# Performance work log

Measured on AMD Instinct MI355X. Metric: run time of the kernel, lower is better.

Reference implementation:

```python
import jax, jax.numpy as jnp
import numpy as np

D_MODEL = 256   # dim // 2
DIM = 512
D_INNER = 512   # expand=2 * d_model
D_STATE = 16
D_CONV = 4
DT_RANK = 16    # ceil(d_model/16)
N_LAYERS = 2
H_RES, W_RES = 16, 16
EPS = 1e-5


def silu(v):
    return v * jax.nn.sigmoid(v)


def setup_inputs() -> dict:
    key = jax.random.key(0)
    ks = jax.random.split(key, 12)
    Bsz, T, N = 2, 4, 256
    x = jax.random.normal(ks[0], (Bsz, 1 + T * N, DIM), jnp.float32)
    skip = jax.random.normal(ks[1], (Bsz, 1 + 4 * T * N, D_MODEL), jnp.float32)
    sc = lambda k, shape, s: jax.random.normal(k, shape, jnp.float32) * s
    exp_w = sc(ks[2], (2 * DIM, DIM), 0.02)            # PatchExpanding2D.expansion (no bias)
    ln_g = jnp.ones((DIM // 2,), jnp.float32)
    ln_b = jnp.zeros((DIM // 2,), jnp.float32)
    cls_w = sc(ks[3], (DIM // 2, DIM), 0.02)
    cls_b = jnp.zeros((DIM // 2,), jnp.float32)
    in_proj_w = sc(ks[4], (N_LAYERS, 2 * D_INNER, D_MODEL), 0.02)
    conv_w = sc(ks[5], (N_LAYERS, D_INNER, D_CONV), 0.1)  # depthwise causal conv
    conv_b = jnp.zeros((N_LAYERS, D_INNER), jnp.float32)
    xproj_w = sc(ks[6], (N_LAYERS, DT_RANK + 2 * D_STATE, D_INNER), 0.02)
    dt_w = sc(ks[7], (N_LAYERS, D_INNER, DT_RANK), 0.1)
    dt_b = sc(ks[8], (N_LAYERS, D_INNER), 0.1)
    A_log = jnp.log(jnp.broadcast_to(jnp.arange(1, D_STATE + 1, dtype=jnp.float32), (N_LAYERS, D_INNER, D_STATE)))
    Dp = jnp.ones((N_LAYERS, D_INNER), jnp.float32)
    out_w = sc(ks[9], (N_LAYERS, D_MODEL, D_INNER), 0.02)
    bn_g = jnp.ones((D_MODEL,), jnp.float32)
    bn_b = jnp.zeros((D_MODEL,), jnp.float32)
    return {"x": x, "skip_connection": skip, "exp_w": exp_w, "ln_g": ln_g, "ln_b": ln_b,
            "cls_w": cls_w, "cls_b": cls_b, "in_proj_w": in_proj_w, "conv_w": conv_w,
            "conv_b": conv_b, "xproj_w": xproj_w, "dt_w": dt_w, "dt_b": dt_b,
            "A_log": A_log, "Dp": Dp, "out_w": out_w, "bn_g": bn_g, "bn_b": bn_b,
            "B": 2, "T": 4, "N": 256}


def mamba_layer(u, Wi, cw, cb, Wx, Wdt, bdt, A_log, Dd, Wo):
    # u: [B, L, d_model]
    Bb, L, _ = u.shape
    xz = jnp.einsum('bld,ed->ble', u, Wi)            # [B, L, 2*d_inner]
    xi, z = jnp.split(xz, 2, axis=-1)
    # depthwise causal conv1d (pad left d_conv-1)
    xp = jnp.pad(xi, ((0, 0), (D_CONV - 1, 0), (0, 0)))
    xc = cb + sum(cw[:, k] * xp[:, k:k + L, :] for k in range(D_CONV))
    xi = silu(xc)
    dbc = jnp.einsum('bld,ed->ble', xi, Wx)          # [B, L, dt_rank + 2*d_state]
    dt = dbc[..., :DT_RANK]
    Bm = dbc[..., DT_RANK:DT_RANK + D_STATE]
    Cm = dbc[..., DT_RANK + D_STATE:]
    delta = jax.nn.softplus(jnp.einsum('blr,dr->bld', dt, Wdt) + bdt)  # [B, L, d_inner]
    A = -jnp.exp(A_log)                              # [d_inner, d_state]

    def step(h, inp):
        d_t, B_t, C_t, x_t = inp                     # [B,d], [B,n], [B,n], [B,d]
        h = h * jnp.exp(d_t[..., None] * A) + d_t[..., None] * B_t[:, None, :] * x_t[..., None]
        y = jnp.einsum('bdn,bn->bd', h, C_t)
        return h, y

    h0 = jnp.zeros((Bb, D_INNER, D_STATE), u.dtype)
    xs = (jnp.swapaxes(delta, 0, 1), jnp.swapaxes(Bm, 0, 1),
          jnp.swapaxes(Cm, 0, 1), jnp.swapaxes(xi, 0, 1))
    _, ys = jax.lax.scan(step, h0, xs)               # ys: [L, B, d_inner]
    y = jnp.swapaxes(ys, 0, 1) + xi * Dd
    y = y * silu(z)
    return jnp.einsum('bld,od->blo', y, Wo)          # [B, L, d_model]


def reference(x, skip_connection, exp_w, ln_g, ln_b, cls_w, cls_b, in_proj_w, conv_w,
              conv_b, xproj_w, dt_w, dt_b, A_log, Dp, out_w, bn_g, bn_b, B, T, N):
    cls = x[:B, :1, :]                               # [B, 1, dim]
    toks = x[:, 1:, :].reshape(x.shape[0], T, N, DIM)
    # patch expanding: Linear dim -> 2*dim, then 2x2 pixel shuffle, LayerNorm(dim//2)
    e = jnp.einsum('btnm,em->btne', toks, exp_w)     # [B, T, N, 2*dim]
    m = (2 * DIM) // 4                               # dim // 2
    e = e.reshape(-1, T, H_RES, W_RES, 2, 2, m)
    e = jnp.transpose(e, (0, 1, 2, 4, 3, 5, 6)).reshape(-1, T, 4 * N, m)
    mu = e.mean(-1, keepdims=True)
    var = e.var(-1, keepdims=True)
    e = (e - mu) / jnp.sqrt(var + EPS) * ln_g + ln_b
    e = e.reshape(e.shape[0], T * 4 * N, m)
    cls = jnp.einsum('bom,em->boe', cls, cls_w) + cls_b
    xx = jnp.concatenate([cls, e], axis=1) + skip_connection
    for i in range(N_LAYERS):
        xx = mamba_layer(xx, in_proj_w[i], conv_w[i], conv_b[i], xproj_w[i],
                         dt_w[i], dt_b[i], A_log[i], Dp[i], out_w[i])
    # BatchNorm1d over channels (training-mode batch stats, biased variance)
    mu = xx.mean(axis=(0, 1))
    var = xx.var(axis=(0, 1))
    xx = (xx - mu) / jnp.sqrt(var + EPS) * bn_g + bn_b
    return xx, 4 * N
```

## Files before the change

kernel.cpp:

```cpp
#include <hip/hip_runtime.h>
#include <hip/hip_bf16.h>
#include <math.h>

#define L_TOT 4097
#define BSZ 2
#define ROWS (BSZ*L_TOT)
#define NSEG 128
#define SEGLEN 33

typedef __bf16 bf16x8 __attribute__((ext_vector_type(8)));
typedef float  f32x4  __attribute__((ext_vector_type(4)));
#define ASTR 56
#define AST2 72

__device__ __forceinline__ float sigmoidf_(float v){ return 1.0f/(1.0f+__expf(-v)); }
__device__ __forceinline__ float siluf_(float v){ return v * sigmoidf_(v); }
__device__ __forceinline__ unsigned short bfbits(float f){
    __bf16 h = (__bf16)f;
    return __builtin_bit_cast(unsigned short, h);
}

__global__ __launch_bounds__(256) void cvt4(
    const float* __restrict__ w0, const float* __restrict__ w1,
    const float* __restrict__ w2, const float* __restrict__ w3,
    __bf16* __restrict__ o0, __bf16* __restrict__ o1,
    __bf16* __restrict__ o2, __bf16* __restrict__ o3)
{
    long i = ((long)blockIdx.x*256 + threadIdx.x)*8;
    const float* src; __bf16* dst; long off;
    if (i < 524288)        { src = w0; dst = o0; off = i; }
    else if (i < 1048576)  { src = w1; dst = o1; off = i - 524288; }
    else if (i < 1310720)  { src = w2; dst = o2; off = i - 1048576; }
    else if (i < 1359872)  { src = w3; dst = o3; off = i - 1310720; }
    else return;
    float4 a = *(const float4*)(src+off), b = *(const float4*)(src+off+4);
    bf16x8 o;
    o[0]=(__bf16)a.x; o[1]=(__bf16)a.y; o[2]=(__bf16)a.z; o[3]=(__bf16)a.w;
    o[4]=(__bf16)b.x; o[5]=(__bf16)b.y; o[6]=(__bf16)b.z; o[7]=(__bf16)b.w;
    *(bf16x8*)(dst+off) = o;
}

__global__ __launch_bounds__(256) void cvt_gather_x(
    const float* __restrict__ x, __bf16* __restrict__ out)
{
    long i = ((long)blockIdx.x*256 + threadIdx.x)*8;
    if (i >= 2048L*512) return;
    int row = (int)(i >> 9), col = (int)(i & 511);
    long srow = row + (row >> 10) + 1;
    const float* src = x + srow*512 + col;
    float4 a = *(const float4*)src, b = *(const float4*)(src+4);
    bf16x8 o;
    o[0]=(__bf16)a.x; o[1]=(__bf16)a.y; o[2]=(__bf16)a.z; o[3]=(__bf16)a.w;
    o[4]=(__bf16)b.x; o[5]=(__bf16)b.y; o[6]=(__bf16)b.z; o[7]=(__bf16)b.w;
    *(bf16x8*)(out+i) = o;
}

__global__ __launch_bounds__(256) void gemm_bf16(
    const __bf16* __restrict__ A, const __bf16* __restrict__ W,
    __bf16* __restrict__ C2, int M, int N, int K)
{
    __shared__ __bf16 Als[128*ASTR];
    __shared__ __bf16 Wls[64*ASTR];
    const int tid = threadIdx.x;
    const int lane = tid & 63, w = tid >> 6;
    const int n0 = blockIdx.x*64, m0 = blockIdx.y*128;

    f32x4 acc[2][4] = {};
    const int arow = tid >> 1, ahalf = tid & 1;
    const int wrow = tid >> 2, wseg = tid & 3;
    const int fr = lane & 15, fc = lane >> 4;

    for (int k0 = 0; k0 < K; k0 += 32) {
        bf16x8 av0 = {}, av1 = {};
        if (m0 + arow < M) {
            const __bf16* src = A + (long)(m0+arow)*K + k0 + ahalf*16;
            av0 = *(const bf16x8*)src;
            av1 = *(const bf16x8*)(src+8);
        }
        bf16x8 wv = *(const bf16x8*)(W + (long)(n0+wrow)*K + k0 + wseg*8);
        __syncthreads();
        *(bf16x8*)&Als[arow*ASTR + ahalf*16]     = av0;
        *(bf16x8*)&Als[arow*ASTR + ahalf*16 + 8] = av1;
        *(bf16x8*)&Wls[wrow*ASTR + wseg*8]       = wv;
        __syncthreads();

        bf16x8 a0 = *(const bf16x8*)&Als[(w*32 +      fr)*ASTR + fc*8];
        bf16x8 a1 = *(const bf16x8*)&Als[(w*32 + 16 + fr)*ASTR + fc*8];
        #pragma unroll
        for (int j = 0; j < 4; j++) {
            bf16x8 bv = *(const bf16x8*)&Wls[(j*16 + fr)*ASTR + fc*8];
            acc[0][j] = __builtin_amdgcn_mfma_f32_16x16x32_bf16(a0, bv, acc[0][j], 0,0,0);
            acc[1][j] = __builtin_amdgcn_mfma_f32_16x16x32_bf16(a1, bv, acc[1][j], 0,0,0);
        }
    }
    #pragma unroll
    for (int i = 0; i < 2; i++) {
        #pragma unroll
        for (int rr = 0; rr < 4; rr++) {
            int grow = m0 + w*32 + i*16 + fc*4 + rr;
            if (grow < M) {
                #pragma unroll
                for (int j = 0; j < 4; j++)
                    C2[(long)grow*N + n0 + j*16 + fr] = (__bf16)acc[i][j][rr];
            }
        }
    }
}

__global__ __launch_bounds__(256) void gemm_inproj(
    const __bf16* __restrict__ A, const __bf16* __restrict__ W,
    __bf16* __restrict__ xhb, __bf16* __restrict__ zsb, int M, int K)
{
    __shared__ __bf16 Als[128*AST2];
    __shared__ __bf16 Wls[128*AST2];
    const int tid = threadIdx.x;
    const int lane = tid & 63, w = tid >> 6;
    const int n0 = blockIdx.x*128, m0 = blockIdx.y*128;
    const int fr = lane & 15, fc = lane >> 4;
    const int row2 = tid >> 1, half = tid & 1;

    f32x4 acc[2][8] = {};

    for (int k0 = 0; k0 < K; k0 += 64) {
        bf16x8 av[4], wv[4];
        const bool aok = (m0 + row2) < M;
        const __bf16* asrc = A + (long)(m0+row2)*K + k0 + half*32;
        const __bf16* wsrc = W + (long)(n0+row2)*K + k0 + half*32;
        #pragma unroll
        for (int e = 0; e < 4; e++) {
            av[e] = aok ? *(const bf16x8*)(asrc + e*8) : (bf16x8){};
            wv[e] = *(const bf16x8*)(wsrc + e*8);
        }
        __syncthreads();
        #pragma unroll
        for (int e = 0; e < 4; e++) {
            *(bf16x8*)&Als[row2*AST2 + half*32 + e*8] = av[e];
            *(bf16x8*)&Wls[row2*AST2 + half*32 + e*8] = wv[e];
        }
        __syncthreads();
        #pragma unroll
        for (int s = 0; s < 2; s++) {
            bf16x8 a0 = *(const bf16x8*)&Als[(w*32 +      fr)*AST2 + s*32 + fc*8];
            bf16x8 a1 = *(const bf16x8*)&Als[(w*32 + 16 + fr)*AST2 + s*32 + fc*8];
            #pragma unroll
            for (int j = 0; j < 8; j++) {
                bf16x8 bv = *(const bf16x8*)&Wls[(j*16 + fr)*AST2 + s*32 + fc*8];
                acc[0][j] = __builtin_amdgcn_mfma_f32_16x16x32_bf16(a0, bv, acc[0][j], 0,0,0);
                acc[1][j] = __builtin_amdgcn_mfma_f32_16x16x32_bf16(a1, bv, acc[1][j], 0,0,0);
            }
        }
    }
    const bool xhalf = (n0 < 512);
    const int cbase = xhalf ? n0 : (n0 - 512);
    #pragma unroll
    for (int i = 0; i < 2; i++) {
        #pragma unroll
        for (int rr = 0; rr < 4; rr++) {
            int grow = m0 + w*32 + i*16 + fc*4 + rr;
            if (grow < M) {
                if (xhalf) {
                    #pragma unroll
                    for (int j = 0; j < 8; j++)
                        xhb[(long)grow*512 + cbase + j*16 + fr] = (__bf16)acc[i][j][rr];
                } else {
                    #pragma unroll
                    for (int j = 0; j < 8; j++)
                        zsb[(long)grow*512 + cbase + j*16 + fr] = (__bf16)siluf_(acc[i][j][rr]);
                }
            }
        }
    }
}

__global__ __launch_bounds__(128) void gemm_dbc(
    const __bf16* __restrict__ A, const __bf16* __restrict__ W,
    float* __restrict__ dt16, float* __restrict__ BC, int M)
{
    __shared__ __bf16 Als[64*ASTR];
    __shared__ __bf16 Wls[48*ASTR];
    const int tid = threadIdx.x;
    const int lane = tid & 63, w = tid >> 6;
    const int m0 = blockIdx.x*64;
    f32x4 acc[2][3] = {};

    const int arow = tid >> 1, ahalf = tid & 1;
    const int fr = lane & 15, fc = lane >> 4;

    for (int k0 = 0; k0 < 512; k0 += 32) {
        bf16x8 av0 = {}, av1 = {};
        if (m0 + arow < M) {
            const __bf16* src = A + (long)(m0+arow)*512 + k0 + ahalf*16;
            av0 = *(const bf16x8*)src;
            av1 = *(const bf16x8*)(src+8);
        }
        bf16x8 wv0 = {}, wv1 = {};
        if (tid < 96) {
            const __bf16* src = W + (long)(tid>>1)*512 + k0 + (tid&1)*16;
            wv0 = *(const bf16x8*)src;
            wv1 = *(const bf16x8*)(src+8);
        }
        __syncthreads();
        *(bf16x8*)&Als[arow*ASTR + ahalf*16]     = av0;
        *(bf16x8*)&Als[arow*ASTR + ahalf*16 + 8] = av1;
        if (tid < 96) {
            *(bf16x8*)&Wls[(tid>>1)*ASTR + (tid&1)*16]     = wv0;
            *(bf16x8*)&Wls[(tid>>1)*ASTR + (tid&1)*16 + 8] = wv1;
        }
        __syncthreads();

        bf16x8 a0 = *(const bf16x8*)&Als[(w*32 +      fr)*ASTR + fc*8];
        bf16x8 a1 = *(const bf16x8*)&Als[(w*32 + 16 + fr)*ASTR + fc*8];
        #pragma unroll
        for (int j = 0; j < 3; j++) {
            bf16x8 bv = *(const bf16x8*)&Wls[(j*16 + fr)*ASTR + fc*8];
            acc[0][j] = __builtin_amdgcn_mfma_f32_16x16x32_bf16(a0, bv, acc[0][j], 0,0,0);
            acc[1][j] = __builtin_amdgcn_mfma_f32_16x16x32_bf16(a1, bv, acc[1][j], 0,0,0);
        }
    }
    #pragma unroll
    for (int i = 0; i < 2; i++) {
        #pragma unroll
        for (int rr = 0; rr < 4; rr++) {
            long grow = m0 + w*32 + i*16 + fc*4 + rr;
            if (grow < M) {
                dt16[grow*16 + fr]    = acc[i][0][rr];
                BC[grow*32 + fr]      = acc[i][1][rr];
                BC[grow*32 + 16 + fr] = acc[i][2][rr];
            }
        }
    }
}

__global__ __launch_bounds__(256) void delta_k(
    const float* __restrict__ dt16, const float* __restrict__ Wdt,
    const float* __restrict__ bdt, const __bf16* __restrict__ xib,
    unsigned* __restrict__ pdx)
{
    __shared__ float dtS[8*16];
    const int tid = threadIdx.x;
    const long r0 = (long)blockIdx.x*8;
    if (tid < 32) {
        long idx = r0*16 + tid*4;
        f32x4 v = (idx < (long)ROWS*16) ? *(const f32x4*)&dt16[idx] : (f32x4){};
        *(f32x4*)&dtS[tid*4] = v;
    }
    const int d0 = tid, d1 = tid + 256;
    f32x4 wa[4], wb[4];
    #pragma unroll
    for (int q = 0; q < 4; q++) {
        wa[q] = *(const f32x4*)(Wdt + d0*16 + q*4);
        wb[q] = *(const f32x4*)(Wdt + d1*16 + q*4);
    }
    const float b0 = bdt[d0], b1 = bdt[d1];
    __syncthreads();
    #pragma unroll
    for (int rr = 0; rr < 8; rr++) {
        long row = r0 + rr;
        if (row >= ROWS) return;
        const float* dt = &dtS[rr*16];
        float s0 = b0, s1 = b1;
        #pragma unroll
        for (int e = 0; e < 4; e++) {
            s0 += wa[0][e]*dt[e] + wa[1][e]*dt[4+e] + wa[2][e]*dt[8+e] + wa[3][e]*dt[12+e];
            s1 += wb[0][e]*dt[e] + wb[1][e]*dt[4+e] + wb[2][e]*dt[8+e] + wb[3][e]*dt[12+e];
        }
        float dl0 = (s0 > 20.f) ? s0 : log1pf(__expf(s0));
        float dl1 = (s1 > 20.f) ? s1 : log1pf(__expf(s1));
        unsigned x0 = __builtin_bit_cast(unsigned short, xib[row*512 + d0]);
        unsigned x1 = __builtin_bit_cast(unsigned short, xib[row*512 + d1]);
        pdx[row*512 + d0] = (unsigned)bfbits(dl0) | (x0 << 16);
        pdx[row*512 + d1] = (unsigned)bfbits(dl1) | (x1 << 16);
    }
}

__global__ __launch_bounds__(256) void cls_k(
    const float* __restrict__ x, const float* __restrict__ cls_w,
    const float* __restrict__ cls_b, const float* __restrict__ skip,
    __bf16* __restrict__ xxb)
{
    const int widx = blockIdx.x*4 + (threadIdx.x >> 6);
    const int lane = threadIdx.x & 63;
    const int b = widx >> 8, c = widx & 255;
    const float* xr = x + (long)b*1025*512 + lane*8;
    const float* wr = cls_w + (long)c*512 + lane*8;
    float4 xa = *(const float4*)xr,      xb4 = *(const float4*)(xr+4);
    float4 wa = *(const float4*)wr,      wb4 = *(const float4*)(wr+4);
    float s = xa.x*wa.x + xa.y*wa.y + xa.z*wa.z + xa.w*wa.w
            + xb4.x*wb4.x + xb4.y*wb4.y + xb4.z*wb4.z + xb4.w*wb4.w;
    #pragma unroll
    for (int o = 32; o > 0; o >>= 1) s += __shfl_xor(s, o);
    if (lane == 0) {
        long o = (long)b*L_TOT*256 + c;
        xxb[o] = (__bf16)(s + cls_b[c] + skip[o]);
    }
}

__global__ __launch_bounds__(256) void rearrange_ln(
    const __bf16* __restrict__ e_buf, const float* __restrict__ ln_g,
    const float* __restrict__ ln_b, const float* __restrict__ skip,
    __bf16* __restrict__ xxb)
{
    const int wv = threadIdx.x >> 6, lane = threadIdx.x & 63;
    const int qg = blockIdx.x*4 + wv;
    const int b = qg >> 12, q = (qg & 4095) + 1;
    const long obase = ((long)b*L_TOT + q)*256;

    const int t  = (q-1) >> 10;
    const int p  = (q-1) & 1023;
    const int h  = p >> 6;
    const int a  = (p >> 5) & 1;
    const int w_ = (p >> 1) & 15;
    const int bb = p & 1;
    const long tok = (long)b*1024 + t*256 + h*16 + w_;
    const __bf16* src = e_buf + tok*1024 + a*512 + bb*256 + lane*4;
    float v[4];
    {
        ushort2 u0 = *(const ushort2*)src;
        ushort2 u1 = *(const ushort2*)(src+2);
        v[0] = (float)__builtin_bit_cast(__bf16, u0.x);
        v[1] = (float)__builtin_bit_cast(__bf16, u0.y);
        v[2] = (float)__builtin_bit_cast(__bf16, u1.x);
        v[3] = (float)__builtin_bit_cast(__bf16, u1.y);
    }
    float s = v[0]+v[1]+v[2]+v[3];
    float s2 = v[0]*v[0]+v[1]*v[1]+v[2]*v[2]+v[3]*v[3];
    #pragma unroll
    for (int o = 32; o > 0; o >>= 1) { s += __shfl_xor(s, o); s2 += __shfl_xor(s2, o); }
    float mu = s * (1.f/256.f);
    float rs = rsqrtf(s2*(1.f/256.f) - mu*mu + 1e-5f);
    const int c0 = lane*4;
    float4 sk = *(const float4*)&skip[obase + c0];
    float skv[4] = {sk.x, sk.y, sk.z, sk.w};
    __bf16 ov[4];
    #pragma unroll
    for (int i = 0; i < 4; i++)
        ov[i] = (__bf16)((v[i] - mu)*rs*ln_g[c0+i] + ln_b[c0+i] + skv[i]);
    *(ushort2*)&xxb[obase + c0]     = make_ushort2(
        __builtin_bit_cast(unsigned short, ov[0]),
        __builtin_bit_cast(unsigned short, ov[1]));
    *(ushort2*)&xxb[obase + c0 + 2] = make_ushort2(
        __builtin_bit_cast(unsigned short, ov[2]),
        __builtin_bit_cast(unsigned short, ov[3]));
}

__global__ __launch_bounds__(256) void conv_silu(
    const __bf16* __restrict__ xhb, const float* __restrict__ cw,
    const float* __restrict__ cb, __bf16* __restrict__ xib)
{
    const int tid = threadIdx.x;
    const int c = tid & 63;
    const long r0 = ((long)blockIdx.x*4 + (tid >> 6))*8;
    if (r0 >= ROWS) return;
    const int d0 = c*8;
    float wreg[4][8], breg[8];
    #pragma unroll
    for (int e = 0; e < 8; e++) {
        breg[e] = cb[d0+e];
        #pragma unroll
        for (int k = 0; k < 4; k++) wreg[k][e] = cw[(d0+e)*4 + k];
    }
    bf16x8 win[4];
    #pragma unroll
    for (int j = 0; j < 3; j++) {
        long rr = r0 - 3 + j;
        win[j] = (rr >= 0) ? *(const bf16x8*)&xhb[rr*512 + d0] : (bf16x8){};
    }
    #pragma unroll
    for (int rr = 0; rr < 8; rr++) {
        long rl = r0 + rr;
        if (rl >= ROWS) break;
        win[3] = *(const bf16x8*)&xhb[rl*512 + d0];
        int l = (int)(rl % L_TOT);
        float acc[8];
        #pragma unroll
        for (int e = 0; e < 8; e++) acc[e] = breg[e];
        #pragma unroll
        for (int k = 0; k < 4; k++) {
            if (l + k - 3 >= 0) {
                #pragma unroll
                for (int e = 0; e < 8; e++)
                    acc[e] += wreg[k][e]*(float)win[k][e];
            }
        }
        bf16x8 o;
        #pragma unroll
        for (int e = 0; e < 8; e++) o[e] = (__bf16)siluf_(acc[e]);
        *(bf16x8*)&xib[rl*512 + d0] = o;
        win[0] = win[1]; win[1] = win[2]; win[2] = win[3];
    }
}

__global__ __launch_bounds__(256) void scan_p1(
    const unsigned* __restrict__ pdx,
    const float* __restrict__ BC, const float* __restrict__ A_log,
    float* __restrict__ segH, float* __restrict__ segP)
{
    __shared__ unsigned pdxS[SEGLEN*64];
    __shared__ float bS[SEGLEN*16];
    const int blk = blockIdx.x;
    const int seg = blk >> 4;
    const int b   = (blk >> 3) & 1;
    const int dbase = (blk & 7)*64;
    const int tid = threadIdx.x;
    const int l0 = seg*SEGLEN;
    const int nl = min(l0 + SEGLEN, L_TOT) - l0;
    const int nlc = nl > 0 ? nl : 0;

    for (int cc = tid; cc < nlc*16; cc += 256) {
        int l = cc >> 4, qq = cc & 15;
        *(uint4*)&pdxS[l*64 + qq*4] =
            *(const uint4*)&pdx[((long)b*L_TOT + l0 + l)*512 + dbase + qq*4];
    }
    for (int cc = tid; cc < nlc*4; cc += 256) {
        int l = cc >> 2, qq = cc & 3;
        *(f32x4*)&bS[l*16 + qq*4] =
            *(const f32x4*)&BC[((long)b*L_TOT + l0 + l)*32 + qq*4];
    }
    __syncthreads();

    const int dl_ = tid >> 2;
    const int d = dbase + dl_;
    const int ng = tid & 3;
    f32x4 Al = *(const f32x4*)(A_log + d*16 + ng*4);
    float Ar[4] = {-__expf(Al[0]), -__expf(Al[1]), -__expf(Al[2]), -__expf(Al[3])};
    float h[4] = {0,0,0,0};
    float P[4] = {1,1,1,1};
    for (int l = 0; l < nlc; l++) {
        unsigned v = pdxS[l*64 + dl_];
        float dl = __uint_as_float(v << 16);
        float xv = __uint_as_float(v & 0xffff0000u);
        f32x4 Bv = *(const f32x4*)&bS[l*16 + ng*4];
        float dx = dl*xv;
        #pragma unroll
        for (int n = 0; n < 4; n++) {
            float E = __expf(dl*Ar[n]);
            h[n] = h[n]*E + dx*Bv[n];
            P[n] *= E;
        }
    }
    long off = ((long)(seg*2 + b)*512 + d)*16 + ng*4;
    *(f32x4*)&segH[off] = f32x4{h[0],h[1],h[2],h[3]};
    *(f32x4*)&segP[off] = f32x4{P[0],P[1],P[2],P[3]};
}

__global__ __launch_bounds__(256) void scan_p2(
    float* __restrict__ segH, const float* __restrict__ segP)
{
    const int idx = blockIdx.x*256 + threadIdx.x;
    float carry = 0.f;
    for (int s0 = 0; s0 < NSEG; s0 += 8) {
        float hh[8], pp[8];
        #pragma unroll
        for (int j = 0; j < 8; j++) {
            long o = (long)(s0+j)*16384 + idx;
            hh[j] = segH[o]; pp[j] = segP[o];
        }
        #pragma unroll
        for (int j = 0; j < 8; j++) {
            long o = (long)(s0+j)*16384 + idx;
            segH[o] = carry;
            carry = pp[j]*carry + hh[j];
        }
    }
}

__global__ __launch_bounds__(256) void scan_p3(
    const unsigned* __restrict__ pdx,
    const float* __restrict__ BC, const float* __restrict__ A_log,
    const float* __restrict__ segH, const float* __restrict__ Dp,
    const __bf16* __restrict__ zsb, __bf16* __restrict__ yb)
{
    __shared__ unsigned pdxS[SEGLEN*64];
    __shared__ float bcS[SEGLEN*32];
    __shared__ __bf16 zS[SEGLEN*64];
    __shared__ __bf16 yS[SEGLEN*64];
    const int blk = blockIdx.x;
    const int seg = blk >> 4;
    const int b   = (blk >> 3) & 1;
    const int dbase = (blk & 7)*64;
    const int tid = threadIdx.x;
    const int l0 = seg*SEGLEN;
    const int nl = min(l0 + SEGLEN, L_TOT) - l0;
    const int nlc = nl > 0 ? nl : 0;
    if (nlc == 0) return;

    for (int cc = tid; cc < nlc*16; cc += 256) {
        int l = cc >> 4, qq = cc & 15;
        *(uint4*)&pdxS[l*64 + qq*4] =
            *(const uint4*)&pdx[((long)b*L_TOT + l0 + l)*512 + dbase + qq*4];
    }
    for (int cc = tid; cc < nlc*8; cc += 256) {
        int l = cc >> 3, qq = cc & 7;
        *(f32x4*)&bcS[l*32 + qq*4] =
            *(const f32x4*)&BC[((long)b*L_TOT + l0 + l)*32 + qq*4];
    }
    for (int cc = tid; cc < nlc*8; cc += 256) {
        int l = cc >> 3, qq = cc & 7;
        *(bf16x8*)&zS[l*64 + qq*8] =
            *(const bf16x8*)&zsb[((long)b*L_TOT + l0 + l)*512 + dbase + qq*8];
    }
    __syncthreads();

    const int dl_ = tid >> 2;
    const int d = dbase + dl_;
    const int ng = tid & 3;
    f32x4 Al = *(const f32x4*)(A_log + d*16 + ng*4);
    float Ar[4] = {-__expf(Al[0]), -__expf(Al[1]), -__expf(Al[2]), -__expf(Al[3])};
    long off = ((long)(seg*2 + b)*512 + d)*16 + ng*4;
    f32x4 h4 = *(const f32x4*)&segH[off];
    float h[4] = {h4[0], h4[1], h4[2], h4[3]};
    const float Dd = Dp[d];
    for (int l = 0; l < nlc; l++) {
        unsigned v = pdxS[l*64 + dl_];
        float dl = __uint_as_float(v << 16);
        float xv = __uint_as_float(v & 0xffff0000u);
        f32x4 Bv = *(const f32x4*)&bcS[l*32 + ng*4];
        f32x4 Cv = *(const f32x4*)&bcS[l*32 + 16 + ng*4];
        float dx = dl*xv;
        float y = 0.f;
        #pragma unroll
        for (int n = 0; n < 4; n++) {
            float E = __expf(dl*Ar[n]);
            h[n] = h[n]*E + dx*Bv[n];
            y += h[n]*Cv[n];
        }
        y += __shfl_xor(y, 1);
        y += __shfl_xor(y, 2);
        if (ng == 0) {
            float z = (float)zS[l*64 + dl_];
            yS[l*64 + dl_] = (__bf16)((y + xv*Dd)*z);
        }
    }
    __syncthreads();
    for (int cc = tid; cc < nlc*8; cc += 256) {
        int l = cc >> 3, qq = cc & 7;
        *(bf16x8*)&yb[((long)b*L_TOT + l0 + l)*512 + dbase + qq*8] =
            *(bf16x8*)&yS[l*64 + qq*8];
    }
}

__global__ void zero_stats(float* __restrict__ stats) { stats[threadIdx.x] = 0.f; }

__global__ __launch_bounds__(256) void bn_reduce(
    const __bf16* __restrict__ xxb, float* __restrict__ stats)
{
    const int c = threadIdx.x;
    float s = 0.f, s2 = 0.f;
    for (int r = blockIdx.x; r < ROWS; r += gridDim.x) {
        float v = (float)xxb[(long)r*256 + c];
        s += v; s2 += v*v;
    }
    atomicAdd(&stats[c], s);
    atomicAdd(&stats[256 + c], s2);
}

__global__ __launch_bounds__(256) void bn_apply(
    const __bf16* __restrict__ xxb, const float* __restrict__ stats,
    const float* __restrict__ g, const float* __restrict__ bta,
    float* __restrict__ out)
{
    long idx = (long)blockIdx.x*256 + threadIdx.x;
    if (idx == 0) out[(long)ROWS*256] = 1024.0f;
    if (idx >= (long)ROWS*256) return;
    int c = (int)(idx & 255);
    float mu = stats[c] * (1.f/ROWS);
    float var = stats[256 + c] * (1.f/ROWS) - mu*mu;
    out[idx] = ((float)xxb[idx] - mu)*rsqrtf(var + 1e-5f)*g[c] + bta[c];
}

extern "C" void kernel_launch(void* const* d_in, const int* in_sizes, int n_in,
                              void* d_out, int out_size, void* d_ws, size_t ws_size,
                              hipStream_t stream)
{
    const float* x        = (const float*)d_in[0];
    const float* skip     = (const float*)d_in[1];
    const float* exp_w    = (const float*)d_in[2];
    const float* ln_g     = (const float*)d_in[3];
    const float* ln_b     = (const float*)d_in[4];
    const float* cls_w    = (const float*)d_in[5];
    const float* cls_b    = (const float*)d_in[6];
    const float* in_proj_w= (const float*)d_in[7];
    const float* conv_w   = (const float*)d_in[8];
    const float* conv_b   = (const float*)d_in[9];
    const float* xproj_w  = (const float*)d_in[10];
    const float* dt_w     = (const float*)d_in[11];
    const float* dt_b     = (const float*)d_in[12];
    const float* A_log    = (const float*)d_in[13];
    const float* Dp       = (const float*)d_in[14];
    const float* out_w    = (const float*)d_in[15];
    const float* bn_g     = (const float*)d_in[16];
    const float* bn_b     = (const float*)d_in[17];

    float* ws = (float*)d_ws;
    float* BC    = ws;
    float* dt16  = BC + 262208;
    float* segH  = dt16 + 131104;
    float* segP  = segH + 2097152;
    float* stats = segP + 2097152;
    unsigned* pdx = (unsigned*)(stats + 512);
    __bf16* expWb = (__bf16*)(pdx + 4195328);
    __bf16* inWb  = expWb + 524288;
    __bf16* outWb = inWb + 524288;
    __bf16* xpWb  = outWb + 262144;
    __bf16* xxb   = xpWb + 49152;
    __bf16* xhb   = xxb + 2097664;
    __bf16* e_b   = xhb;
    __bf16* zsb   = xhb + 4195328;
    __bf16* xib   = zsb + 4195328;
    __bf16* Axb   = xib;
    __bf16* yb    = xib + 4195328;
    float* out    = (float*)d_out;

    cvt4<<<(1359872/8 + 255)/256, 256, 0, stream>>>(
        exp_w, in_proj_w, out_w, xproj_w, expWb, inWb, outWb, xpWb);
    cvt_gather_x<<<(1048576/8)/256, 256, 0, stream>>>(x, Axb);

    gemm_bf16<<<dim3(16, 16), 256, 0, stream>>>(
        Axb, expWb, e_b, 2048, 1024, 512);
    cls_k<<<128, 256, 0, stream>>>(x, cls_w, cls_b, skip, xxb);
    rearrange_ln<<<2048, 256, 0, stream>>>(e_b, ln_g, ln_b, skip, xxb);

    for (int layer = 0; layer < 2; layer++) {
        gemm_inproj<<<dim3(8, 65), 256, 0, stream>>>(
            xxb, inWb + layer*262144, xhb, zsb, ROWS, 256);
        conv_silu<<<(ROWS + 31)/32, 256, 0, stream>>>(
            xhb, conv_w + layer*512*4, conv_b + layer*512, xib);
        gemm_dbc<<<(ROWS + 63)/64, 128, 0, stream>>>(
            xib, xpWb + layer*24576, dt16, BC, ROWS);
        delta_k<<<(ROWS + 7)/8, 256, 0, stream>>>(
            dt16, dt_w + layer*512*16, dt_b + layer*512, xib, pdx);
        scan_p1<<<NSEG*16, 256, 0, stream>>>(
            pdx, BC, A_log + layer*512*16, segH, segP);
        scan_p2<<<64, 256, 0, stream>>>(segH, segP);
        scan_p3<<<NSEG*16, 256, 0, stream>>>(
            pdx, BC, A_log + layer*512*16, segH, Dp + layer*512, zsb, yb);
        gemm_bf16<<<dim3(4, 65), 256, 0, stream>>>(
            yb, outWb + layer*131072, xxb, ROWS, 256, 512);
    }

    zero_stats<<<1, 512, 0, stream>>>(stats);
    bn_reduce<<<128, 256, 0, stream>>>(xxb, stats);
    bn_apply<<<((long)ROWS*256 + 255)/256 + 1, 256, 0, stream>>>(
        xxb, stats, bn_g, bn_b, out);
}
```

Before: 392.0 us.

## Fuse prep/cls kernels, halve scan segments, widen dbc GEMM, reuse scan shared memory

Merges the weight conversion, x gather and stats zeroing into one prep kernel, and folds the cls projection into the rearrange+LayerNorm kernel, which cuts the number of launches. The scan now uses 64 segments of 65 steps instead of 128 of 33, so there is less segment-carry work but more serial length per segment. The x-projection GEMM moves to 256 threads with one 16-row tile per wave. Scan phase 3 writes its output into the pdx shared buffer and drops yS to save LDS. Several unrelated changes are bundled, and the segment-length change shifts the balance between scan parallelism and carry overhead.

```diff
diff --git a/kernel.cpp b/kernel.cpp
--- a/kernel.cpp
+++ b/kernel.cpp
@@ -5,8 +5,8 @@
 #define L_TOT 4097
 #define BSZ 2
 #define ROWS (BSZ*L_TOT)
-#define NSEG 128
-#define SEGLEN 33
+#define NSEG 64
+#define SEGLEN 65
 
 typedef __bf16 bf16x8 __attribute__((ext_vector_type(8)));
 typedef float  f32x4  __attribute__((ext_vector_type(4)));
@@ -20,30 +20,34 @@
     return __builtin_bit_cast(unsigned short, h);
 }
 
-__global__ __launch_bounds__(256) void cvt4(
+__global__ __launch_bounds__(256) void prep_all(
     const float* __restrict__ w0, const float* __restrict__ w1,
     const float* __restrict__ w2, const float* __restrict__ w3,
+    const float* __restrict__ x,
     __bf16* __restrict__ o0, __bf16* __restrict__ o1,
-    __bf16* __restrict__ o2, __bf16* __restrict__ o3)
-{
-    long i = ((long)blockIdx.x*256 + threadIdx.x)*8;
-    const float* src; __bf16* dst; long off;
-    if (i < 524288)        { src = w0; dst = o0; off = i; }
-    else if (i < 1048576)  { src = w1; dst = o1; off = i - 524288; }
-    else if (i < 1310720)  { src = w2; dst = o2; off = i - 1048576; }
-    else if (i < 1359872)  { src = w3; dst = o3; off = i - 1310720; }
-    else return;
-    float4 a = *(const float4*)(src+off), b = *(const float4*)(src+off+4);
-    bf16x8 o;
-    o[0]=(__bf16)a.x; o[1]=(__bf16)a.y; o[2]=(__bf16)a.z; o[3]=(__bf16)a.w;
-    o[4]=(__bf16)b.x; o[5]=(__bf16)b.y; o[6]=(__bf16)b.z; o[7]=(__bf16)b.w;
-    *(bf16x8*)(dst+off) = o;
-}
-
-__global__ __launch_bounds__(256) void cvt_gather_x(
-    const float* __restrict__ x, __bf16* __restrict__ out)
-{
-    long i = ((long)blockIdx.x*256 + threadIdx.x)*8;
+    __bf16* __restrict__ o2, __bf16* __restrict__ o3,
+    __bf16* __restrict__ gx, float* __restrict__ stats)
+{
+    const int bid = blockIdx.x;
+    if (bid < 664) {
+        long i = ((long)bid*256 + threadIdx.x)*8;
+        const float* src; __bf16* dst; long off;
+        if (i < 524288)        { src = w0; dst = o0; off = i; }
+        else if (i < 1048576)  { src = w1; dst = o1; off = i - 524288; }
+        else if (i < 1310720)  { src = w2; dst = o2; off = i - 1048576; }
+        else                   { src = w3; dst = o3; off = i - 1310720; }
+        float4 a = *(const float4*)(src+off), b = *(const float4*)(src+off+4);
+        bf16x8 o;
+        o[0]=(__bf16)a.x; o[1]=(__bf16)a.y; o[2]=(__bf16)a.z; o[3]=(__bf16)a.w;
+        o[4]=(__bf16)b.x; o[5]=(__bf16)b.y; o[6]=(__bf16)b.z; o[7]=(__bf16)b.w;
+        *(bf16x8*)(dst+off) = o;
+        return;
+    }
+    if (bid == 664) {
+        stats[threadIdx.x] = 0.f;
+        stats[threadIdx.x + 256] = 0.f;
+    }
+    long i = ((long)(bid-664)*256 + threadIdx.x)*8;
     if (i >= 2048L*512) return;
     int row = (int)(i >> 9), col = (int)(i & 511);
     long srow = row + (row >> 10) + 1;
@@ -52,7 +56,7 @@
     bf16x8 o;
     o[0]=(__bf16)a.x; o[1]=(__bf16)a.y; o[2]=(__bf16)a.z; o[3]=(__bf16)a.w;
     o[4]=(__bf16)b.x; o[5]=(__bf16)b.y; o[6]=(__bf16)b.z; o[7]=(__bf16)b.w;
-    *(bf16x8*)(out+i) = o;
+    *(bf16x8*)(gx+i) = o;
 }
 
 __global__ __launch_bounds__(256) void gemm_bf16(
@@ -172,7 +176,7 @@
     }
 }
 
-__global__ __launch_bounds__(128) void gemm_dbc(
+__global__ __launch_bounds__(256) void gemm_dbc(
     const __bf16* __restrict__ A, const __bf16* __restrict__ W,
     float* __restrict__ dt16, float* __restrict__ BC, int M)
 {
@@ -181,52 +185,37 @@
     const int tid = threadIdx.x;
     const int lane = tid & 63, w = tid >> 6;
     const int m0 = blockIdx.x*64;
-    f32x4 acc[2][3] = {};
-
-    const int arow = tid >> 1, ahalf = tid & 1;
+    f32x4 acc[3] = {};
+
+    const int arow = tid >> 2, aseg = tid & 3;
     const int fr = lane & 15, fc = lane >> 4;
 
     for (int k0 = 0; k0 < 512; k0 += 32) {
-        bf16x8 av0 = {}, av1 = {};
-        if (m0 + arow < M) {
-            const __bf16* src = A + (long)(m0+arow)*512 + k0 + ahalf*16;
-            av0 = *(const bf16x8*)src;
-            av1 = *(const bf16x8*)(src+8);
-        }
-        bf16x8 wv0 = {}, wv1 = {};
-        if (tid < 96) {
-            const __bf16* src = W + (long)(tid>>1)*512 + k0 + (tid&1)*16;
-            wv0 = *(const bf16x8*)src;
-            wv1 = *(const bf16x8*)(src+8);
-        }
+        bf16x8 av = {};
+        if (m0 + arow < M)
+            av = *(const bf16x8*)(A + (long)(m0+arow)*512 + k0 + aseg*8);
+        bf16x8 wv = {};
+        if (tid < 192)
+            wv = *(const bf16x8*)(W + (long)(tid>>2)*512 + k0 + (tid&3)*8);
         __syncthreads();
-        *(bf16x8*)&Als[arow*ASTR + ahalf*16]     = av0;
-        *(bf16x8*)&Als[arow*ASTR + ahalf*16 + 8] = av1;
-        if (tid < 96) {
-            *(bf16x8*)&Wls[(tid>>1)*ASTR + (tid&1)*16]     = wv0;
-            *(bf16x8*)&Wls[(tid>>1)*ASTR + (tid&1)*16 + 8] = wv1;
-        }
+        *(bf16x8*)&Als[arow*ASTR + aseg*8] = av;
+        if (tid < 192) *(bf16x8*)&Wls[(tid>>2)*ASTR + (tid&3)*8] = wv;
         __syncthreads();
 
-        bf16x8 a0 = *(const bf16x8*)&Als[(w*32 +      fr)*ASTR + fc*8];
-        bf16x8 a1 = *(const bf16x8*)&Als[(w*32 + 16 + fr)*ASTR + fc*8];
+        bf16x8 a0 = *(const bf16x8*)&Als[(w*16 + fr)*ASTR + fc*8];
         #pragma unroll
         for (int j = 0; j < 3; j++) {
             bf16x8 bv = *(const bf16x8*)&Wls[(j*16 + fr)*ASTR + fc*8];
-            acc[0][j] = __builtin_amdgcn_mfma_f32_16x16x32_bf16(a0, bv, acc[0][j], 0,0,0);
-            acc[1][j] = __builtin_amdgcn_mfma_f32_16x16x32_bf16(a1, bv, acc[1][j], 0,0,0);
-        }
-    }
-    #pragma unroll
-    for (int i = 0; i < 2; i++) {
-        #pragma unroll
-        for (int rr = 0; rr < 4; rr++) {
-            long grow = m0 + w*32 + i*16 + fc*4 + rr;
-            if (grow < M) {
-                dt16[grow*16 + fr]    = acc[i][0][rr];
-                BC[grow*32 + fr]      = acc[i][1][rr];
-                BC[grow*32 + 16 + fr] = acc[i][2][rr];
-            }
+            acc[j] = __builtin_amdgcn_mfma_f32_16x16x32_bf16(a0, bv, acc[j], 0,0,0);
+        }
+    }
+    #pragma unroll
+    for (int rr = 0; rr < 4; rr++) {
+        long grow = m0 + w*16 + fc*4 + rr;
+        if (grow < M) {
+            dt16[grow*16 + fr]    = acc[0][rr];
+            BC[grow*32 + fr]      = acc[1][rr];
+            BC[grow*32 + 16 + fr] = acc[2][rr];
         }
     }
 }
@@ -273,34 +262,30 @@
     }
 }
 
-__global__ __launch_bounds__(256) void cls_k(
-    const float* __restrict__ x, const float* __restrict__ cls_w,
-    const float* __restrict__ cls_b, const float* __restrict__ skip,
-    __bf16* __restrict__ xxb)
-{
-    const int widx = blockIdx.x*4 + (threadIdx.x >> 6);
-    const int lane = threadIdx.x & 63;
-    const int b = widx >> 8, c = widx & 255;
-    const float* xr = x + (long)b*1025*512 + lane*8;
-    const float* wr = cls_w + (long)c*512 + lane*8;
-    float4 xa = *(const float4*)xr,      xb4 = *(const float4*)(xr+4);
-    float4 wa = *(const float4*)wr,      wb4 = *(const float4*)(wr+4);
-    float s = xa.x*wa.x + xa.y*wa.y + xa.z*wa.z + xa.w*wa.w
-            + xb4.x*wb4.x + xb4.y*wb4.y + xb4.z*wb4.z + xb4.w*wb4.w;
-    #pragma unroll
-    for (int o = 32; o > 0; o >>= 1) s += __shfl_xor(s, o);
-    if (lane == 0) {
-        long o = (long)b*L_TOT*256 + c;
-        xxb[o] = (__bf16)(s + cls_b[c] + skip[o]);
-    }
-}
-
-__global__ __launch_bounds__(256) void rearrange_ln(
-    const __bf16* __restrict__ e_buf, const float* __restrict__ ln_g,
-    const float* __restrict__ ln_b, const float* __restrict__ skip,
-    __bf16* __restrict__ xxb)
+__global__ __launch_bounds__(256) void rearrange_ln_cls(
+    const __bf16* __restrict__ e_buf, const float* __restrict__ x,
+    const float* __restrict__ cls_w, const float* __restrict__ cls_b,
+    const float* __restrict__ ln_g, const float* __restrict__ ln_b,
+    const float* __restrict__ skip, __bf16* __restrict__ xxb)
 {
     const int wv = threadIdx.x >> 6, lane = threadIdx.x & 63;
+    if (blockIdx.x >= 2048) {
+        const int widx = (blockIdx.x - 2048)*4 + wv;
+        const int b = widx >> 8, c = widx & 255;
+        const float* xr = x + (long)b*1025*512 + lane*8;
+        const float* wr = cls_w + (long)c*512 + lane*8;
+        float4 xa = *(const float4*)xr,  xb4 = *(const float4*)(xr+4);
+        float4 wa = *(const float4*)wr,  wb4 = *(const float4*)(wr+4);
+        float s = xa.x*wa.x + xa.y*wa.y + xa.z*wa.z + xa.w*wa.w
+                + xb4.x*wb4.x + xb4.y*wb4.y + xb4.z*wb4.z + xb4.w*wb4.w;
+        #pragma unroll
+        for (int o = 32; o > 0; o >>= 1) s += __shfl_xor(s, o);
+        if (lane == 0) {
+            long o = (long)b*L_TOT*256 + c;
+            xxb[o] = (__bf16)(s + cls_b[c] + skip[o]);
+        }
+        return;
+    }
     const int qg = blockIdx.x*4 + wv;
     const int b = qg >> 12, q = (qg & 4095) + 1;
     const long obase = ((long)b*L_TOT + q)*256;
@@ -473,7 +458,6 @@
     __shared__ unsigned pdxS[SEGLEN*64];
     __shared__ float bcS[SEGLEN*32];
     __shared__ __bf16 zS[SEGLEN*64];
-    __shared__ __bf16 yS[SEGLEN*64];
     const int blk = blockIdx.x;
     const int seg = blk >> 4;
     const int b   = (blk >> 3) & 1;
@@ -528,18 +512,20 @@
         y += __shfl_xor(y, 2);
         if (ng == 0) {
             float z = (float)zS[l*64 + dl_];
-            yS[l*64 + dl_] = (__bf16)((y + xv*Dd)*z);
+            ((unsigned short*)&pdxS[l*64 + dl_])[0] = bfbits((y + xv*Dd)*z);
         }
     }
     __syncthreads();
     for (int cc = tid; cc < nlc*8; cc += 256) {
         int l = cc >> 3, qq = cc & 7;
-        *(bf16x8*)&yb[((long)b*L_TOT + l0 + l)*512 + dbase + qq*8] =
-            *(bf16x8*)&yS[l*64 + qq*8];
-    }
-}
-
-__global__ void zero_stats(float* __restrict__ stats) { stats[threadIdx.x] = 0.f; }
+        bf16x8 o;
+        #pragma unroll
+        for (int e = 0; e < 8; e++)
+            o[e] = __builtin_bit_cast(__bf16,
+                       (unsigned short)(pdxS[l*64 + qq*8 + e] & 0xffffu));
+        *(bf16x8*)&yb[((long)b*L_TOT + l0 + l)*512 + dbase + qq*8] = o;
+    }
+}
 
 __global__ __launch_bounds__(256) void bn_reduce(
     const __bf16* __restrict__ xxb, float* __restrict__ stats)
@@ -595,8 +581,8 @@
     float* BC    = ws;
     float* dt16  = BC + 262208;
     float* segH  = dt16 + 131104;
-    float* segP  = segH + 2097152;
-    float* stats = segP + 2097152;
+    float* segP  = segH + 1048576;
+    float* stats = segP + 1048576;
     unsigned* pdx = (unsigned*)(stats + 512);
     __bf16* expWb = (__bf16*)(pdx + 4195328);
     __bf16* inWb  = expWb + 524288;
@@ -611,21 +597,21 @@
     __bf16* yb    = xib + 4195328;
     float* out    = (float*)d_out;
 
-    cvt4<<<(1359872/8 + 255)/256, 256, 0, stream>>>(
-        exp_w, in_proj_w, out_w, xproj_w, expWb, inWb, outWb, xpWb);
-    cvt_gather_x<<<(1048576/8)/256, 256, 0, stream>>>(x, Axb);
+    prep_all<<<1176, 256, 0, stream>>>(
+        exp_w, in_proj_w, out_w, xproj_w, x,
+        expWb, inWb, outWb, xpWb, Axb, stats);
 
     gemm_bf16<<<dim3(16, 16), 256, 0, stream>>>(
         Axb, expWb, e_b, 2048, 1024, 512);
-    cls_k<<<128, 256, 0, stream>>>(x, cls_w, cls_b, skip, xxb);
-    rearrange_ln<<<2048, 256, 0, stream>>>(e_b, ln_g, ln_b, skip, xxb);
+    rearrange_ln_cls<<<2176, 256, 0, stream>>>(
+        e_b, x, cls_w, cls_b, ln_g, ln_b, skip, xxb);
 
     for (int layer = 0; layer < 2; layer++) {
         gemm_inproj<<<dim3(8, 65), 256, 0, stream>>>(
             xxb, inWb + layer*262144, xhb, zsb, ROWS, 256);
         conv_silu<<<(ROWS + 31)/32, 256, 0, stream>>>(
             xhb, conv_w + layer*512*4, conv_b + layer*512, xib);
-        gemm_dbc<<<(ROWS + 63)/64, 128, 0, stream>>>(
+        gemm_dbc<<<(ROWS + 63)/64, 256, 0, stream>>>(
             xib, xpWb + layer*24576, dt16, BC, ROWS);
         delta_k<<<(ROWS + 7)/8, 256, 0, stream>>>(
             dt16, dt_w + layer*512*16, dt_b + layer*512, xib, pdx);
@@ -638,7 +624,6 @@
             yb, outWb + layer*131072, xxb, ROWS, 256, 512);
     }
 
-    zero_stats<<<1, 512, 0, stream>>>(stats);
     bn_reduce<<<128, 256, 0, stream>>>(xxb, stats);
     bn_apply<<<((long)ROWS*256 + 255)/256 + 1, 256, 0, stream>>>(
         xxb, stats, bn_g, bn_b, out);
```

Result: faster. 376.7 us (-3.9%).
